# Kernel tuning notes

Hardware: AMD Instinct MI355X
Metric: run time of the kernel (lower is better)

The kernel has to match this reference:

```python
import jax, jax.numpy as jnp
import numpy as np

B, LEADS, T = 256, 12, 2250
ENC_DIM = 768           # encoder.width
LATENT = 128            # latent_dim
K = 512                 # num_embeddings
COMMIT = 0.1            # commitment_cost
IN_DIM = LEADS * T      # 27000


def setup_inputs() -> dict:
    key = jax.random.key(0)
    ks = jax.random.split(key, 9)
    s = lambda d: 1.0 / np.sqrt(d)
    return {
        "x": jax.random.normal(ks[0], (B, LEADS, T), dtype=jnp.float32),
        # frozen pretrained encoder, modeled as a linear projection (stop_gradient in reference)
        "W_enc": jax.random.normal(ks[1], (IN_DIM, ENC_DIM), dtype=jnp.float32) * s(IN_DIM),
        # to_latent
        "W_lat": jax.random.normal(ks[2], (ENC_DIM, LATENT), dtype=jnp.float32) * s(ENC_DIM),
        "b_lat": jnp.zeros((LATENT,), dtype=jnp.float32),
        # VQ codebook: torch.rand - 0.5  -> uniform(-0.5, 0.5)
        "codebook": jax.random.uniform(ks[3], (K, LATENT), dtype=jnp.float32, minval=-0.5, maxval=0.5),
        # decoder: Linear(LATENT, ENC_DIM) -> ReLU -> Linear(ENC_DIM, IN_DIM)
        "W_d1": jax.random.normal(ks[4], (LATENT, ENC_DIM), dtype=jnp.float32) * s(LATENT),
        "b_d1": jnp.zeros((ENC_DIM,), dtype=jnp.float32),
        "W_d2": jax.random.normal(ks[5], (ENC_DIM, IN_DIM), dtype=jnp.float32) * s(ENC_DIM),
        "b_d2": jnp.zeros((IN_DIM,), dtype=jnp.float32),
    }


def _vq(z, codebook):
    # z: [B, D]; codebook: [K, D]
    # distances = |z|^2 + |e|^2 - 2 z e^T   -> [B, K]
    d = (jnp.sum(z * z, axis=1, keepdims=True)
         + jnp.sum(codebook * codebook, axis=1)
         - 2.0 * jnp.matmul(z, codebook.T))
    idx = jnp.argmin(d, axis=1)                 # [B]
    quant = codebook[idx]                       # gather [B, D]
    e_latent = jnp.mean((jax.lax.stop_gradient(quant) - z) ** 2)
    q_latent = jnp.mean((quant - jax.lax.stop_gradient(z)) ** 2)
    loss = q_latent + COMMIT * e_latent
    quant_st = z + jax.lax.stop_gradient(quant - z)   # straight-through
    return quant_st, loss, idx


def reference(x, W_enc, W_lat, b_lat, codebook, W_d1, b_d1, W_d2, b_d2):
    # frozen encoder (requires_grad=False / torch.no_grad)
    features = jax.lax.stop_gradient(x.reshape(x.shape[0], -1) @ W_enc)   # [B, ENC_DIM]
    z = features @ W_lat + b_lat                                          # [B, LATENT]
    z_q, vq_loss, indices = _vq(z, codebook)
    h = jax.nn.relu(z_q @ W_d1 + b_d1)
    x_recon = (h @ W_d2 + b_d2).reshape(-1, LEADS, T)                     # [B, 12, 2250]
    recon_loss = jnp.mean((x_recon - x) ** 2)
    return x_recon, recon_loss + vq_loss, vq_loss, indices
```

## Files before the change

kernel.cpp:

```cpp
#include <hip/hip_runtime.h>
#include <hip/hip_bf16.h>

#define IN_DIM   27000
#define ENC_DIM  768
#define LATENT   128
#define K_CODES  512
#define BATCH    256
#define ZCH      288
#define NZC      94
#define NWC      422
#define BN_R     64
#define NRB      422
#define PADK     40
#define NKT      24

#define OUT_WCTH_US   0
#define OUT_WCTL_US   (128*IN_DIM)
#define OUT_ZPART_F   (128*IN_DIM)

#define WS_Z      0
#define WS_QUANT  (WS_Z + BATCH*LATENT)
#define WS_IDX    (WS_QUANT + BATCH*LATENT)
#define WS_VQPART (WS_IDX + BATCH)
#define WS_RECON  (WS_VQPART + BATCH)
#define WS_HBF    (WS_RECON + 1024)
#define WS_WLH    (WS_HBF + 49152)
#define WS_WLL    (WS_WLH + 49152)

typedef unsigned short ushort_t;
typedef __attribute__((ext_vector_type(4))) float f32x4;
typedef __attribute__((ext_vector_type(8))) short short8x;
typedef __attribute__((ext_vector_type(4))) short short4x;

__device__ __forceinline__ ushort_t bf16_rne(float f) {
    unsigned u = __float_as_uint(f);
    unsigned r = 0x7FFFu + ((u >> 16) & 1u);
    return (ushort_t)((u + r) >> 16);
}
__device__ __forceinline__ void split_f32(float v, ushort_t& h, ushort_t& l) {
    unsigned u  = __float_as_uint(v);
    unsigned uh = u & 0xFFFF0000u;
    h = (ushort_t)(uh >> 16);
    l = bf16_rne(v - __uint_as_float(uh));
}
__device__ __forceinline__ void lds_barrier() {
    asm volatile("s_waitcnt lgkmcnt(0)\n\ts_barrier" ::: "memory");
}

__global__ __launch_bounds__(256) void k_prep(const float* __restrict__ Wlat,
                                              ushort_t* __restrict__ wlh,
                                              ushort_t* __restrict__ wll) {
    const int i4 = blockIdx.x * 256 + threadIdx.x;
    const int k  = i4 >> 5;
    const int n4 = (i4 & 31) * 4;
    float4 v = *(const float4*)(Wlat + (size_t)k * LATENT + n4);
    float vv[4] = {v.x, v.y, v.z, v.w};
#pragma unroll
    for (int j = 0; j < 4; j++) {
        ushort_t h, l;
        split_f32(vv[j], h, l);
        wlh[(size_t)(n4 + j) * ENC_DIM + k] = h;
        wll[(size_t)(n4 + j) * ENC_DIM + k] = l;
    }
}

__global__ __launch_bounds__(256) void k_wc(const float* __restrict__ Wenc,
                                            const ushort_t* __restrict__ wlh,
                                            const ushort_t* __restrict__ wll,
                                            ushort_t* __restrict__ wcth,
                                            ushort_t* __restrict__ wctl) {
    __shared__ ushort_t Ah[2][64][PADK], Al[2][64][PADK];
    __shared__ ushort_t Bh[2][128][PADK], Bl[2][128][PADK];
    const int t = threadIdx.x, lane = t & 63, w = t >> 6;
    const int lrow = lane & 15, kg = lane >> 4;
    const int m0 = blockIdx.x * 64;

    const int a_row = t >> 3, a_kq = t & 7;
    const int b_n   = t >> 2, b_ck = t & 3;

    float4  areg0[2], areg1[2];
    short8x bhreg0[2], blreg0[2], bhreg1[2], blreg1[2];

    f32x4 acc[8];
#pragma unroll
    for (int ni = 0; ni < 8; ni++) acc[ni] = (f32x4){0.f, 0.f, 0.f, 0.f};

#define WC_LOAD(S, kt)                                                          \
    {                                                                           \
        const int k0_ = (kt) * 32;                                              \
        _Pragma("unroll")                                                       \
        for (int p = 0; p < 2; p++) {                                           \
            int r = m0 + a_row + p * 32; if (r > IN_DIM - 1) r = IN_DIM - 1;    \
            areg##S[p] = *(const float4*)(Wenc + (size_t)r * ENC_DIM + k0_ + a_kq * 4); \
        }                                                                       \
        _Pragma("unroll")                                                       \
        for (int p = 0; p < 2; p++) {                                           \
            const size_t bo = (size_t)(b_n + p * 64) * ENC_DIM + k0_ + b_ck * 8;\
            bhreg##S[p] = *(const short8x*)(wlh + bo);                          \
            blreg##S[p] = *(const short8x*)(wll + bo);                          \
        }                                                                       \
    }
#define WC_STORE(S, BI)                                                         \
    {                                                                           \
        _Pragma("unroll")                                                       \
        for (int p = 0; p < 2; p++) {                                           \
            const int row = a_row + p * 32;                                     \
            float vv[4] = {areg##S[p].x, areg##S[p].y, areg##S[p].z, areg##S[p].w}; \
            short4x h4, l4;                                                     \
            _Pragma("unroll")                                                   \
            for (int i = 0; i < 4; i++) {                                       \
                ushort_t h, l; split_f32(vv[i], h, l);                          \
                h4[i] = (short)h; l4[i] = (short)l;                             \
            }                                                                   \
            *(short4x*)&Ah[BI][row][a_kq * 4] = h4;                             \
            *(short4x*)&Al[BI][row][a_kq * 4] = l4;                             \
        }                                                                       \
        _Pragma("unroll")                                                       \
        for (int p = 0; p < 2; p++) {                                           \
            const int n = b_n + p * 64;                                         \
            *(short8x*)&Bh[BI][n][b_ck * 8] = bhreg##S[p];                      \
            *(short8x*)&Bl[BI][n][b_ck * 8] = blreg##S[p];                      \
        }                                                                       \
    }
#define WC_MFMA(BI)                                                             \
    {                                                                           \
        short8x ah = *(const short8x*)&Ah[BI][w * 16 + lrow][kg * 8];           \
        short8x al = *(const short8x*)&Al[BI][w * 16 + lrow][kg * 8];           \
        _Pragma("unroll")                                                       \
        for (int ni = 0; ni < 8; ni++) {                                        \
            short8x bhf = *(const short8x*)&Bh[BI][ni * 16 + lrow][kg * 8];     \
            short8x blf = *(const short8x*)&Bl[BI][ni * 16 + lrow][kg * 8];     \
            acc[ni] = __builtin_amdgcn_mfma_f32_16x16x32_bf16(ah, bhf, acc[ni], 0, 0, 0); \
            acc[ni] = __builtin_amdgcn_mfma_f32_16x16x32_bf16(ah, blf, acc[ni], 0, 0, 0); \
            acc[ni] = __builtin_amdgcn_mfma_f32_16x16x32_bf16(al, bhf, acc[ni], 0, 0, 0); \
        }                                                                       \
    }

    const int NT = NKT;
    WC_LOAD(0, 0)
    WC_LOAD(1, 1)
    WC_STORE(0, 0)
    lds_barrier();

    for (int kt = 0; kt < NT; kt += 2) {
        if (kt + 2 < NT) WC_LOAD(0, kt + 2)
        WC_MFMA(0)
        WC_STORE(1, 1)
        lds_barrier();
        if (kt + 3 < NT) WC_LOAD(1, kt + 3)
        WC_MFMA(1)
        if (kt + 2 < NT) WC_STORE(0, 0)
        lds_barrier();
    }
#undef WC_LOAD
#undef WC_STORE
#undef WC_MFMA

    const int rowb = m0 + w * 16 + kg * 4;
    if (rowb < IN_DIM) {
#pragma unroll
        for (int ni = 0; ni < 8; ni++) {
            const int col = ni * 16 + lrow;
            short4x h4, l4;
#pragma unroll
            for (int r = 0; r < 4; r++) {
                ushort_t h, l; split_f32(acc[ni][r], h, l);
                h4[r] = (short)h; l4[r] = (short)l;
            }
            *(short4x*)(wcth + (size_t)col * IN_DIM + rowb) = h4;
            *(short4x*)(wctl + (size_t)col * IN_DIM + rowb) = l4;
        }
    }
}

__global__ __launch_bounds__(256) void k_z(const float* __restrict__ x,
                                           const ushort_t* __restrict__ wcth,
                                           const ushort_t* __restrict__ wctl,
                                           float* __restrict__ zpart) {
    __shared__ ushort_t Ah[2][64][PADK], Al[2][64][PADK];
    __shared__ ushort_t Bh[2][128][PADK], Bl[2][128][PADK];
    const int t = threadIdx.x, lane = t & 63, w = t >> 6;
    const int lrow = lane & 15, kg = lane >> 4;
    const int m0 = blockIdx.x * 64;
    const int c  = blockIdx.y;
    const int kb = c * ZCH;
    const int k_end = min(IN_DIM, kb + ZCH);
    const int nt = (k_end - kb + 31) >> 5;

    const int a_row = t >> 3, a_kq = t & 7;
    const int b_n   = t >> 2, b_ck = t & 3;

    float4  areg0[2], areg1[2];
    short8x bhreg0[2], blreg0[2], bhreg1[2], blreg1[2];

    f32x4 acc[8];
#pragma unroll
    for (int ni = 0; ni < 8; ni++) acc[ni] = (f32x4){0.f, 0.f, 0.f, 0.f};

#define Z_LOAD(S, kt)                                                           \
    {                                                                           \
        const int k0_ = kb + (kt) * 32;                                         \
        _Pragma("unroll")                                                       \
        for (int p = 0; p < 2; p++) {                                           \
            const int kk = k0_ + a_kq * 4;                                      \
            if (kk < k_end) {                                                   \
                const int r = m0 + a_row + p * 32;                              \
                areg##S[p] = *(const float4*)(x + (size_t)r * IN_DIM + kk);     \
            } else {                                                            \
                areg##S[p] = (float4){0.f, 0.f, 0.f, 0.f};                      \
            }                                                                   \
        }                                                                       \
        _Pragma("unroll")                                                       \
        for (int p = 0; p < 2; p++) {                                           \
            const int kk = k0_ + b_ck * 8;                                      \
            if (kk < k_end) {                                                   \
                const size_t bo = (size_t)(b_n + p * 64) * IN_DIM + kk;         \
                bhreg##S[p] = *(const short8x*)(wcth + bo);                     \
                blreg##S[p] = *(const short8x*)(wctl + bo);                     \
            } else {                                                            \
                short8x zz = {0, 0, 0, 0, 0, 0, 0, 0};                          \
                bhreg##S[p] = zz; blreg##S[p] = zz;                             \
            }                                                                   \
        }                                                                       \
    }
#define Z_STORE(S, BI)                                                          \
    {                                                                           \
        _Pragma("unroll")                                                       \
        for (int p = 0; p < 2; p++) {                                           \
            const int row = a_row + p * 32;                                     \
            float vv[4] = {areg##S[p].x, areg##S[p].y, areg##S[p].z, areg##S[p].w}; \
            short4x h4, l4;                                                     \
            _Pragma("unroll")                                                   \
            for (int i = 0; i < 4; i++) {                                       \
                ushort_t h, l; split_f32(vv[i], h, l);                          \
                h4[i] = (short)h; l4[i] = (short)l;                             \
            }                                                                   \
            *(short4x*)&Ah[BI][row][a_kq * 4] = h4;                             \
            *(short4x*)&Al[BI][row][a_kq * 4] = l4;                             \
        }                                                                       \
        _Pragma("unroll")                                                       \
        for (int p = 0; p < 2; p++) {                                           \
            const int n = b_n + p * 64;                                         \
            *(short8x*)&Bh[BI][n][b_ck * 8] = bhreg##S[p];                      \
            *(short8x*)&Bl[BI][n][b_ck * 8] = blreg##S[p];                      \
        }                                                                       \
    }
#define Z_MFMA(BI)                                                              \
    {                                                                           \
        short8x ah = *(const short8x*)&Ah[BI][w * 16 + lrow][kg * 8];           \
        short8x al = *(const short8x*)&Al[BI][w * 16 + lrow][kg * 8];           \
        _Pragma("unroll")                                                       \
        for (int ni = 0; ni < 8; ni++) {                                        \
            short8x bhf = *(const short8x*)&Bh[BI][ni * 16 + lrow][kg * 8];     \
            short8x blf = *(const short8x*)&Bl[BI][ni * 16 + lrow][kg * 8];     \
            acc[ni] = __builtin_amdgcn_mfma_f32_16x16x32_bf16(ah, bhf, acc[ni], 0, 0, 0); \
            acc[ni] = __builtin_amdgcn_mfma_f32_16x16x32_bf16(ah, blf, acc[ni], 0, 0, 0); \
            acc[ni] = __builtin_amdgcn_mfma_f32_16x16x32_bf16(al, bhf, acc[ni], 0, 0, 0); \
        }                                                                       \
    }

    Z_LOAD(0, 0)
    if (nt > 1) Z_LOAD(1, 1)
    Z_STORE(0, 0)
    lds_barrier();

    for (int kt = 0; kt < nt; kt += 2) {
        if (kt + 2 < nt) Z_LOAD(0, kt + 2)
        Z_MFMA(0)
        if (kt + 1 < nt) Z_STORE(1, 1)
        lds_barrier();
        if (kt + 1 < nt) {
            if (kt + 3 < nt) Z_LOAD(1, kt + 3)
            Z_MFMA(1)
            if (kt + 2 < nt) Z_STORE(0, 0)
            lds_barrier();
        }
    }
#undef Z_LOAD
#undef Z_STORE
#undef Z_MFMA

    float* zp = zpart + (size_t)c * (BATCH * LATENT);
    const int rowb = m0 + w * 16 + kg * 4;
#pragma unroll
    for (int ni = 0; ni < 8; ni++) {
        const int col = ni * 16 + lrow;
#pragma unroll
        for (int r = 0; r < 4; r++)
            zp[(size_t)(rowb + r) * LATENT + col] = acc[ni][r];
    }
}

__global__ __launch_bounds__(256) void k_zred(const float* __restrict__ zpart,
                                              const float* __restrict__ blat,
                                              float* __restrict__ z) {
    const int o = blockIdx.x * 256 + threadIdx.x;
    float s = blat[o & (LATENT - 1)];
    for (int c = 0; c < NZC; c++) s += zpart[(size_t)c * (BATCH * LATENT) + o];
    z[o] = s;
}

__global__ __launch_bounds__(256) void k_vq(const float* __restrict__ z,
                                            const float* __restrict__ cb,
                                            float* __restrict__ quant,
                                            int* __restrict__ idx_out,
                                            float* __restrict__ vqpart) {
    __shared__ float zs[LATENT];
    __shared__ float ds_[256];
    __shared__ int   is_[256];
    const int b = blockIdx.x, t = threadIdx.x;
    if (t < LATENT) zs[t] = z[b * LATENT + t];
    __syncthreads();

    float best_d = 3.4e38f; int best_i = 0;
#pragma unroll
    for (int rep = 0; rep < 2; rep++) {
        const int k = t + rep * 256;
        const float* e = cb + (size_t)k * LATENT;
        float acc = 0.f;
#pragma unroll 4
        for (int d = 0; d < LATENT; d += 4) {
            float4 ev = *(const float4*)(e + d);
            float d0 = zs[d]   - ev.x;
            float d1 = zs[d+1] - ev.y;
            float d2 = zs[d+2] - ev.z;
            float d3 = zs[d+3] - ev.w;
            acc += d0*d0 + d1*d1 + d2*d2 + d3*d3;
        }
        if (acc < best_d) { best_d = acc; best_i = k; }
    }
    ds_[t] = best_d; is_[t] = best_i;
    __syncthreads();
    for (int s = 128; s > 0; s >>= 1) {
        if (t < s) {
            float od = ds_[t+s]; int oi = is_[t+s];
            if (od < ds_[t] || (od == ds_[t] && oi < is_[t])) { ds_[t] = od; is_[t] = oi; }
        }
        __syncthreads();
    }
    const int best = is_[0];
    if (t == 0) idx_out[b] = best;

    float sq = 0.f;
    if (t < LATENT) {
        float q = cb[(size_t)best * LATENT + t];
        quant[b * LATENT + t] = q;
        float dd = q - zs[t];
        sq = dd * dd;
    }
    __syncthreads();
    ds_[t] = sq;
    __syncthreads();
    for (int s = 128; s > 0; s >>= 1) {
        if (t < s) ds_[t] += ds_[t+s];
        __syncthreads();
    }
    if (t == 0) vqpart[b] = ds_[0];
}

__global__ __launch_bounds__(256) void k_h(const float* __restrict__ quant,
                                           const float* __restrict__ Wd1,
                                           const float* __restrict__ bd1,
                                           ushort_t* __restrict__ hfrag) {
    const int bid = blockIdx.x, t = threadIdx.x;
    const int row = bid / 3;
    const int col = (bid % 3) * 256 + t;
    float acc = bd1[col];
    const float* q = quant + row * LATENT;
#pragma unroll 8
    for (int k = 0; k < LATENT; k++)
        acc = fmaf(q[k], Wd1[(size_t)k * ENC_DIM + col], acc);
    const int mt = row >> 4, lrow = row & 15;
    const int kt = col >> 5, kg = (col & 31) >> 3, j = col & 7;
    hfrag[((size_t)(mt * NKT + kt) * 64 + kg * 16 + lrow) * 8 + j] =
        bf16_rne(fmaxf(acc, 0.f));
}

__global__ __launch_bounds__(512) void k_recon_mfma(const ushort_t* __restrict__ hfrag,
                                                    const float* __restrict__ Wd2,
                                                    const float* __restrict__ bd2,
                                                    const float* __restrict__ x,
                                                    float* __restrict__ out,
                                                    float* __restrict__ reconpart) {
    __shared__ ushort_t Bts[2][BN_R][PADK];
    __shared__ float red[512];
    const int t = threadIdx.x, lane = t & 63, wid = t >> 6;
    const int lrow = lane & 15, kg = lane >> 4;
    const int n0 = blockIdx.x * BN_R;

    const int b_n   = lane;
    const int b_kq  = wid;
    const bool bvalid = (n0 + b_n) < IN_DIM;
    const ushort_t* afrag0 = hfrag + ((size_t)(wid * 2 + 0) * NKT * 64 + lane) * 8;
    const ushort_t* afrag1 = hfrag + ((size_t)(wid * 2 + 1) * NKT * 64 + lane) * 8;

    f32x4 acc[2][4];
#pragma unroll
    for (int mi = 0; mi < 2; mi++)
#pragma unroll
        for (int ni = 0; ni < 4; ni++) acc[mi][ni] = (f32x4){0.f, 0.f, 0.f, 0.f};

    short8x a0[2], a1[2], a2[2], a3[2];
    float   bregs0[4], bregs1[4], bregs2[4], bregs3[4];

#define R_ALOAD(S, kt)                                                          \
    {                                                                           \
        a##S[0] = *(const short8x*)(afrag0 + (size_t)(kt) * 512);               \
        a##S[1] = *(const short8x*)(afrag1 + (size_t)(kt) * 512);               \
    }
#define R_BLOAD(S, kt)                                                          \
    {                                                                           \
        if (bvalid) {                                                           \
            const float* wp = Wd2 + (size_t)((kt) * 32 + b_kq * 4) * IN_DIM + n0 + b_n; \
            _Pragma("unroll")                                                   \
            for (int j = 0; j < 4; j++) bregs##S[j] = wp[(size_t)j * IN_DIM];   \
        } else {                                                                \
            _Pragma("unroll")                                                   \
            for (int j = 0; j < 4; j++) bregs##S[j] = 0.f;                      \
        }                                                                       \
    }
#define R_BSTORE(S, BI)                                                         \
    {                                                                           \
        short4x bb;                                                             \
        _Pragma("unroll")                                                       \
        for (int j = 0; j < 4; j++) bb[j] = (short)bf16_rne(bregs##S[j]);       \
        *(short4x*)&Bts[BI][b_n][b_kq * 4] = bb;                                \
    }
#define R_MFMA(S, BI)                                                           \
    {                                                                           \
        short8x b_[4];                                                          \
        _Pragma("unroll")                                                       \
        for (int ni = 0; ni < 4; ni++)                                          \
            b_[ni] = *(const short8x*)&Bts[BI][ni * 16 + lrow][kg * 8];         \
        _Pragma("unroll")                                                       \
        for (int mi = 0; mi < 2; mi++)                                          \
            _Pragma("unroll")                                                   \
            for (int ni = 0; ni < 4; ni++)                                      \
                acc[mi][ni] = __builtin_amdgcn_mfma_f32_16x16x32_bf16(a##S[mi], b_[ni], acc[mi][ni], 0, 0, 0); \
    }

    R_ALOAD(0, 0) R_BLOAD(0, 0)
    R_ALOAD(1, 1) R_BLOAD(1, 1)
    R_ALOAD(2, 2) R_BLOAD(2, 2)
    R_BSTORE(0, 0)
    lds_barrier();

    for (int kt0 = 0; kt0 < NKT; kt0 += 4) {
        if (kt0 + 3 < NKT) { R_ALOAD(3, kt0 + 3) R_BLOAD(3, kt0 + 3) }
        R_MFMA(0, 0)
        if (kt0 + 1 < NKT) R_BSTORE(1, 1)
        lds_barrier();
        if (kt0 + 4 < NKT) { R_ALOAD(0, kt0 + 4) R_BLOAD(0, kt0 + 4) }
        R_MFMA(1, 1)
        if (kt0 + 2 < NKT) R_BSTORE(2, 0)
        lds_barrier();
        if (kt0 + 5 < NKT) { R_ALOAD(1, kt0 + 5) R_BLOAD(1, kt0 + 5) }
        R_MFMA(2, 0)
        if (kt0 + 3 < NKT) R_BSTORE(3, 1)
        lds_barrier();
        if (kt0 + 6 < NKT) { R_ALOAD(2, kt0 + 6) R_BLOAD(2, kt0 + 6) }
        R_MFMA(3, 1)
        if (kt0 + 4 < NKT) R_BSTORE(0, 0)
        lds_barrier();
    }
#undef R_ALOAD
#undef R_BLOAD
#undef R_BSTORE
#undef R_MFMA

    float lsq = 0.f;
#pragma unroll
    for (int mi = 0; mi < 2; mi++) {
        const int rowb = wid * 32 + mi * 16 + kg * 4;
#pragma unroll
        for (int ni = 0; ni < 4; ni++) {
            const int col = n0 + ni * 16 + lrow;
            if (col < IN_DIM) {
                const float bb = bd2[col];
#pragma unroll
                for (int r = 0; r < 4; r++) {
                    const int row = rowb + r;
                    float v = acc[mi][ni][r] + bb;
                    float e = v - x[(size_t)row * IN_DIM + col];
                    lsq += e * e;
                    out[(size_t)row * IN_DIM + col] = v;
                }
            }
        }
    }

    red[t] = lsq;
    __syncthreads();
    for (int s = 256; s > 0; s >>= 1) {
        if (t < s) red[t] += red[t + s];
        __syncthreads();
    }
    if (t == 0) reconpart[blockIdx.x] = red[0];
}

__global__ __launch_bounds__(256) void k_final(const float* __restrict__ reconpart,
                                               const float* __restrict__ vqpart,
                                               const int* __restrict__ idx,
                                               float* __restrict__ out,
                                               long long obase) {
    __shared__ float red[256];
    const int t = threadIdx.x;
    float s = 0.f;
    for (int i = t; i < NRB; i += 256) s += reconpart[i];
    red[t] = s;
    __syncthreads();
    for (int st = 128; st > 0; st >>= 1) {
        if (t < st) red[t] += red[t + st];
        __syncthreads();
    }
    const float recon_sum = red[0];
    __syncthreads();
    red[t] = vqpart[t];
    __syncthreads();
    for (int st = 128; st > 0; st >>= 1) {
        if (t < st) red[t] += red[t + st];
        __syncthreads();
    }
    const float vq_sum = red[0];
    if (t == 0) {
        float recon_loss = recon_sum / (float)((size_t)BATCH * IN_DIM);
        float vq_loss = 1.1f * vq_sum / (float)(BATCH * LATENT);
        out[obase + 0] = recon_loss + vq_loss;
        out[obase + 1] = vq_loss;
    }
    out[obase + 2 + t] = (float)idx[t];
}

extern "C" void kernel_launch(void* const* d_in, const int* in_sizes, int n_in,
                              void* d_out, int out_size, void* d_ws, size_t ws_size,
                              hipStream_t stream) {
    int ix = 0, iwe = 1, iwl = 2, ibl = 3, icb = 4, iwd1 = 5, ibd1 = 6, iwd2 = 7, ibd2 = 8;
    if (n_in == 9 && in_sizes[0] != BATCH * IN_DIM) {
        int p20[2] = {1, 7}, n20 = 0, p98[2] = {2, 5}, n98 = 0;
        for (int i = 0; i < 9; i++) {
            const int s = in_sizes[i];
            if      (s == BATCH * IN_DIM)    ix = i;
            else if (s == LATENT)            ibl = i;
            else if (s == K_CODES * LATENT)  icb = i;
            else if (s == ENC_DIM)           ibd1 = i;
            else if (s == IN_DIM)            ibd2 = i;
            else if (s == IN_DIM * ENC_DIM)  { if (n20 < 2) p20[n20++] = i; }
            else if (s == ENC_DIM * LATENT)  { if (n98 < 2) p98[n98++] = i; }
        }
        iwd2 = p20[0]; iwe = p20[1];
        iwd1 = p98[0]; iwl = p98[1];
    }
    const float* x    = (const float*)d_in[ix];
    const float* Wenc = (const float*)d_in[iwe];
    const float* Wlat = (const float*)d_in[iwl];
    const float* blat = (const float*)d_in[ibl];
    const float* cb   = (const float*)d_in[icb];
    const float* Wd1  = (const float*)d_in[iwd1];
    const float* bd1  = (const float*)d_in[ibd1];
    const float* Wd2  = (const float*)d_in[iwd2];
    const float* bd2  = (const float*)d_in[ibd2];

    float* out = (float*)d_out;
    ushort_t* wcth  = (ushort_t*)d_out + OUT_WCTH_US;
    ushort_t* wctl  = (ushort_t*)d_out + OUT_WCTL_US;
    float*    zpart = out + OUT_ZPART_F;

    float* ws            = (float*)d_ws;
    float* z             = ws + WS_Z;
    float* quant         = ws + WS_QUANT;
    int*   idxp          = (int*)(ws + WS_IDX);
    float* vqpart        = ws + WS_VQPART;
    float* reconpart     = ws + WS_RECON;
    ushort_t* hfrag      = (ushort_t*)(ws + WS_HBF);
    ushort_t* wlh        = (ushort_t*)(ws + WS_WLH);
    ushort_t* wll        = (ushort_t*)(ws + WS_WLL);

    const long long obase = (long long)out_size - 258;

    k_prep      <<<96, 256, 0, stream>>>(Wlat, wlh, wll);
    k_wc        <<<NWC, 256, 0, stream>>>(Wenc, wlh, wll, wcth, wctl);
    k_z         <<<dim3(4, NZC), 256, 0, stream>>>(x, wcth, wctl, zpart);
    k_zred      <<<128, 256, 0, stream>>>(zpart, blat, z);
    k_vq        <<<BATCH, 256, 0, stream>>>(z, cb, quant, idxp, vqpart);
    k_h         <<<768, 256, 0, stream>>>(quant, Wd1, bd1, hfrag);
    k_recon_mfma<<<NRB, 512, 0, stream>>>(hfrag, Wd2, bd2, x, out, reconpart);
    k_final     <<<1, 256, 0, stream>>>(reconpart, vqpart, idxp, out, obase);
}
```

Before: 128.8 us.

## Load A operand directly into MFMA registers, skipping LDS staging in k_wc and k_z

In both the W_enc×W_lat precompute kernel and the x×Wc GEMM, the A operand (fp32 rows) is now read straight from global memory into the per-lane MFMA fragment layout and split to bf16 hi/lo in registers, instead of being staged through shared memory. A is prefetched three k-tiles ahead with a 4-deep register ring, while B keeps double-buffered LDS staging. This removes the A LDS writes and reads and halves shared memory use, at the cost of more registers and less coalesced per-lane global loads (32 contiguous bytes per lane).

```diff
diff --git a/kernel.cpp b/kernel.cpp
--- a/kernel.cpp
+++ b/kernel.cpp
@@ -69,63 +69,49 @@
                                             const ushort_t* __restrict__ wll,
                                             ushort_t* __restrict__ wcth,
                                             ushort_t* __restrict__ wctl) {
-    __shared__ ushort_t Ah[2][64][PADK], Al[2][64][PADK];
     __shared__ ushort_t Bh[2][128][PADK], Bl[2][128][PADK];
     const int t = threadIdx.x, lane = t & 63, w = t >> 6;
     const int lrow = lane & 15, kg = lane >> 4;
     const int m0 = blockIdx.x * 64;
-
-    const int a_row = t >> 3, a_kq = t & 7;
-    const int b_n   = t >> 2, b_ck = t & 3;
-
-    float4  areg0[2], areg1[2];
-    short8x bhreg0[2], blreg0[2], bhreg1[2], blreg1[2];
+    int arow = m0 + w * 16 + lrow; if (arow > IN_DIM - 1) arow = IN_DIM - 1;
+    const float* aptr = Wenc + (size_t)arow * ENC_DIM + kg * 8;
+    const int bn = t >> 1, bkc = (t & 1) * 16;
+    const size_t bbase = (size_t)bn * ENC_DIM + bkc;
 
     f32x4 acc[8];
 #pragma unroll
     for (int ni = 0; ni < 8; ni++) acc[ni] = (f32x4){0.f, 0.f, 0.f, 0.f};
 
-#define WC_LOAD(S, kt)                                                          \
-    {                                                                           \
-        const int k0_ = (kt) * 32;                                              \
-        _Pragma("unroll")                                                       \
-        for (int p = 0; p < 2; p++) {                                           \
-            int r = m0 + a_row + p * 32; if (r > IN_DIM - 1) r = IN_DIM - 1;    \
-            areg##S[p] = *(const float4*)(Wenc + (size_t)r * ENC_DIM + k0_ + a_kq * 4); \
+    float av0[8], av1[8], av2[8], av3[8];
+    short8x bh0[2], bl0[2], bh1[2], bl1[2];
+
+#define WC_ALOAD(S, kt)                                                         \
+    {                                                                           \
+        *(float4*)&av##S[0] = *(const float4*)(aptr + (kt) * 32);               \
+        *(float4*)&av##S[4] = *(const float4*)(aptr + (kt) * 32 + 4);           \
+    }
+#define WC_BLOAD(S, kt)                                                         \
+    {                                                                           \
+        const ushort_t* ph = wlh + bbase + (kt) * 32;                           \
+        const ushort_t* pl = wll + bbase + (kt) * 32;                           \
+        bh##S[0] = *(const short8x*)ph;   bh##S[1] = *(const short8x*)(ph + 8); \
+        bl##S[0] = *(const short8x*)pl;   bl##S[1] = *(const short8x*)(pl + 8); \
+    }
+#define WC_BSTORE(S, BI)                                                        \
+    {                                                                           \
+        *(short8x*)&Bh[BI][bn][bkc]     = bh##S[0];                             \
+        *(short8x*)&Bh[BI][bn][bkc + 8] = bh##S[1];                             \
+        *(short8x*)&Bl[BI][bn][bkc]     = bl##S[0];                             \
+        *(short8x*)&Bl[BI][bn][bkc + 8] = bl##S[1];                             \
+    }
+#define WC_MFMA(S, BI)                                                          \
+    {                                                                           \
+        short8x ah, al;                                                         \
+        _Pragma("unroll")                                                       \
+        for (int i = 0; i < 8; i++) {                                           \
+            ushort_t h, l; split_f32(av##S[i], h, l);                           \
+            ah[i] = (short)h; al[i] = (short)l;                                 \
         }                                                                       \
-        _Pragma("unroll")                                                       \
-        for (int p = 0; p < 2; p++) {                                           \
-            const size_t bo = (size_t)(b_n + p * 64) * ENC_DIM + k0_ + b_ck * 8;\
-            bhreg##S[p] = *(const short8x*)(wlh + bo);                          \
-            blreg##S[p] = *(const short8x*)(wll + bo);                          \
-        }                                                                       \
-    }
-#define WC_STORE(S, BI)                                                         \
-    {                                                                           \
-        _Pragma("unroll")                                                       \
-        for (int p = 0; p < 2; p++) {                                           \
-            const int row = a_row + p * 32;                                     \
-            float vv[4] = {areg##S[p].x, areg##S[p].y, areg##S[p].z, areg##S[p].w}; \
-            short4x h4, l4;                                                     \
-            _Pragma("unroll")                                                   \
-            for (int i = 0; i < 4; i++) {                                       \
-                ushort_t h, l; split_f32(vv[i], h, l);                          \
-                h4[i] = (short)h; l4[i] = (short)l;                             \
-            }                                                                   \
-            *(short4x*)&Ah[BI][row][a_kq * 4] = h4;                             \
-            *(short4x*)&Al[BI][row][a_kq * 4] = l4;                             \
-        }                                                                       \
-        _Pragma("unroll")                                                       \
-        for (int p = 0; p < 2; p++) {                                           \
-            const int n = b_n + p * 64;                                         \
-            *(short8x*)&Bh[BI][n][b_ck * 8] = bhreg##S[p];                      \
-            *(short8x*)&Bl[BI][n][b_ck * 8] = blreg##S[p];                      \
-        }                                                                       \
-    }
-#define WC_MFMA(BI)                                                             \
-    {                                                                           \
-        short8x ah = *(const short8x*)&Ah[BI][w * 16 + lrow][kg * 8];           \
-        short8x al = *(const short8x*)&Al[BI][w * 16 + lrow][kg * 8];           \
         _Pragma("unroll")                                                       \
         for (int ni = 0; ni < 8; ni++) {                                        \
             short8x bhf = *(const short8x*)&Bh[BI][ni * 16 + lrow][kg * 8];     \
@@ -136,24 +122,36 @@
         }                                                                       \
     }
 
-    const int NT = NKT;
-    WC_LOAD(0, 0)
-    WC_LOAD(1, 1)
-    WC_STORE(0, 0)
+    WC_ALOAD(0, 0) WC_ALOAD(1, 1) WC_ALOAD(2, 2)
+    WC_BLOAD(0, 0) WC_BLOAD(1, 1)
+    WC_BSTORE(0, 0)
     lds_barrier();
 
-    for (int kt = 0; kt < NT; kt += 2) {
-        if (kt + 2 < NT) WC_LOAD(0, kt + 2)
-        WC_MFMA(0)
-        WC_STORE(1, 1)
-        lds_barrier();
-        if (kt + 3 < NT) WC_LOAD(1, kt + 3)
-        WC_MFMA(1)
-        if (kt + 2 < NT) WC_STORE(0, 0)
-        lds_barrier();
-    }
-#undef WC_LOAD
-#undef WC_STORE
+    for (int kt0 = 0; kt0 < NKT; kt0 += 4) {
+        if (kt0 + 3 < NKT) WC_ALOAD(3, kt0 + 3)
+        if (kt0 + 2 < NKT) WC_BLOAD(0, kt0 + 2)
+        WC_MFMA(0, 0)
+        if (kt0 + 1 < NKT) WC_BSTORE(1, 1)
+        lds_barrier();
+        if (kt0 + 4 < NKT) WC_ALOAD(0, kt0 + 4)
+        if (kt0 + 3 < NKT) WC_BLOAD(1, kt0 + 3)
+        WC_MFMA(1, 1)
+        if (kt0 + 2 < NKT) WC_BSTORE(0, 0)
+        lds_barrier();
+        if (kt0 + 5 < NKT) WC_ALOAD(1, kt0 + 5)
+        if (kt0 + 4 < NKT) WC_BLOAD(0, kt0 + 4)
+        WC_MFMA(2, 0)
+        if (kt0 + 3 < NKT) WC_BSTORE(1, 1)
+        lds_barrier();
+        if (kt0 + 6 < NKT) WC_ALOAD(2, kt0 + 6)
+        if (kt0 + 5 < NKT) WC_BLOAD(1, kt0 + 5)
+        WC_MFMA(3, 1)
+        if (kt0 + 4 < NKT) WC_BSTORE(0, 0)
+        lds_barrier();
+    }
+#undef WC_ALOAD
+#undef WC_BLOAD
+#undef WC_BSTORE
 #undef WC_MFMA
 
     const int rowb = m0 + w * 16 + kg * 4;
@@ -177,7 +175,6 @@
                                            const ushort_t* __restrict__ wcth,
                                            const ushort_t* __restrict__ wctl,
                                            float* __restrict__ zpart) {
-    __shared__ ushort_t Ah[2][64][PADK], Al[2][64][PADK];
     __shared__ ushort_t Bh[2][128][PADK], Bl[2][128][PADK];
     const int t = threadIdx.x, lane = t & 63, w = t >> 6;
     const int lrow = lane & 15, kg = lane >> 4;
@@ -187,68 +184,55 @@
     const int k_end = min(IN_DIM, kb + ZCH);
     const int nt = (k_end - kb + 31) >> 5;
 
-    const int a_row = t >> 3, a_kq = t & 7;
-    const int b_n   = t >> 2, b_ck = t & 3;
-
-    float4  areg0[2], areg1[2];
-    short8x bhreg0[2], blreg0[2], bhreg1[2], blreg1[2];
+    const float* aptr = x + (size_t)(m0 + w * 16 + lrow) * IN_DIM + kb + kg * 8;
+    const int bn = t >> 1, bkc = (t & 1) * 16;
+    const size_t bbase = (size_t)bn * IN_DIM + kb + bkc;
 
     f32x4 acc[8];
 #pragma unroll
     for (int ni = 0; ni < 8; ni++) acc[ni] = (f32x4){0.f, 0.f, 0.f, 0.f};
 
-#define Z_LOAD(S, kt)                                                           \
-    {                                                                           \
-        const int k0_ = kb + (kt) * 32;                                         \
-        _Pragma("unroll")                                                       \
-        for (int p = 0; p < 2; p++) {                                           \
-            const int kk = k0_ + a_kq * 4;                                      \
-            if (kk < k_end) {                                                   \
-                const int r = m0 + a_row + p * 32;                              \
-                areg##S[p] = *(const float4*)(x + (size_t)r * IN_DIM + kk);     \
-            } else {                                                            \
-                areg##S[p] = (float4){0.f, 0.f, 0.f, 0.f};                      \
-            }                                                                   \
+    float av0[8], av1[8], av2[8], av3[8];
+    short8x bh0[2], bl0[2], bh1[2], bl1[2];
+
+#define Z_ALOAD(S, kt)                                                          \
+    {                                                                           \
+        if (kb + (kt) * 32 + kg * 8 < k_end) {                                  \
+            *(float4*)&av##S[0] = *(const float4*)(aptr + (kt) * 32);           \
+            *(float4*)&av##S[4] = *(const float4*)(aptr + (kt) * 32 + 4);       \
+        } else {                                                                \
+            _Pragma("unroll")                                                   \
+            for (int i = 0; i < 8; i++) av##S[i] = 0.f;                         \
         }                                                                       \
-        _Pragma("unroll")                                                       \
-        for (int p = 0; p < 2; p++) {                                           \
-            const int kk = k0_ + b_ck * 8;                                      \
-            if (kk < k_end) {                                                   \
-                const size_t bo = (size_t)(b_n + p * 64) * IN_DIM + kk;         \
-                bhreg##S[p] = *(const short8x*)(wcth + bo);                     \
-                blreg##S[p] = *(const short8x*)(wctl + bo);                     \
-            } else {                                                            \
-                short8x zz = {0, 0, 0, 0, 0, 0, 0, 0};                          \
-                bhreg##S[p] = zz; blreg##S[p] = zz;                             \
-            }                                                                   \
+    }
+#define Z_BLOAD(S, kt)                                                          \
+    {                                                                           \
+        const int ko = kb + (kt) * 32 + bkc;                                    \
+        const ushort_t* ph = wcth + bbase + (kt) * 32;                          \
+        const ushort_t* pl = wctl + bbase + (kt) * 32;                          \
+        const short8x zz = {0, 0, 0, 0, 0, 0, 0, 0};                            \
+        if (ko < k_end)     { bh##S[0] = *(const short8x*)ph;                   \
+                              bl##S[0] = *(const short8x*)pl; }                 \
+        else                { bh##S[0] = zz; bl##S[0] = zz; }                   \
+        if (ko + 8 < k_end) { bh##S[1] = *(const short8x*)(ph + 8);             \
+                              bl##S[1] = *(const short8x*)(pl + 8); }           \
+        else                { bh##S[1] = zz; bl##S[1] = zz; }                   \
+    }
+#define Z_BSTORE(S, BI)                                                         \
+    {                                                                           \
+        *(short8x*)&Bh[BI][bn][bkc]     = bh##S[0];                             \
+        *(short8x*)&Bh[BI][bn][bkc + 8] = bh##S[1];                             \
+        *(short8x*)&Bl[BI][bn][bkc]     = bl##S[0];                             \
+        *(short8x*)&Bl[BI][bn][bkc + 8] = bl##S[1];                             \
+    }
+#define Z_MFMA(S, BI)                                                           \
+    {                                                                           \
+        short8x ah, al;                                                         \
+        _Pragma("unroll")                                                       \
+        for (int i = 0; i < 8; i++) {                                           \
+            ushort_t h, l; split_f32(av##S[i], h, l);                           \
+            ah[i] = (short)h; al[i] = (short)l;                                 \
         }                                                                       \
-    }
-#define Z_STORE(S, BI)                                                          \
-    {                                                                           \
-        _Pragma("unroll")                                                       \
-        for (int p = 0; p < 2; p++) {                                           \
-            const int row = a_row + p * 32;                                     \
-            float vv[4] = {areg##S[p].x, areg##S[p].y, areg##S[p].z, areg##S[p].w}; \
-            short4x h4, l4;                                                     \
-            _Pragma("unroll")                                                   \
-            for (int i = 0; i < 4; i++) {                                       \
-                ushort_t h, l; split_f32(vv[i], h, l);                          \
-                h4[i] = (short)h; l4[i] = (short)l;                             \
-            }                                                                   \
-            *(short4x*)&Ah[BI][row][a_kq * 4] = h4;                             \
-            *(short4x*)&Al[BI][row][a_kq * 4] = l4;                             \
-        }                                                                       \
-        _Pragma("unroll")                                                       \
-        for (int p = 0; p < 2; p++) {                                           \
-            const int n = b_n + p * 64;                                         \
-            *(short8x*)&Bh[BI][n][b_ck * 8] = bhreg##S[p];                      \
-            *(short8x*)&Bl[BI][n][b_ck * 8] = blreg##S[p];                      \
-        }                                                                       \
-    }
-#define Z_MFMA(BI)                                                              \
-    {                                                                           \
-        short8x ah = *(const short8x*)&Ah[BI][w * 16 + lrow][kg * 8];           \
-        short8x al = *(const short8x*)&Al[BI][w * 16 + lrow][kg * 8];           \
         _Pragma("unroll")                                                       \
         for (int ni = 0; ni < 8; ni++) {                                        \
             short8x bhf = *(const short8x*)&Bh[BI][ni * 16 + lrow][kg * 8];     \
@@ -259,25 +243,44 @@
         }                                                                       \
     }
 
-    Z_LOAD(0, 0)
-    if (nt > 1) Z_LOAD(1, 1)
-    Z_STORE(0, 0)
+    Z_ALOAD(0, 0) Z_ALOAD(1, 1) Z_ALOAD(2, 2)
+    Z_BLOAD(0, 0) Z_BLOAD(1, 1)
+    Z_BSTORE(0, 0)
     lds_barrier();
 
-    for (int kt = 0; kt < nt; kt += 2) {
-        if (kt + 2 < nt) Z_LOAD(0, kt + 2)
-        Z_MFMA(0)
-        if (kt + 1 < nt) Z_STORE(1, 1)
-        lds_barrier();
-        if (kt + 1 < nt) {
-            if (kt + 3 < nt) Z_LOAD(1, kt + 3)
-            Z_MFMA(1)
-            if (kt + 2 < nt) Z_STORE(0, 0)
+    for (int kt0 = 0; kt0 < nt; kt0 += 4) {
+        if (kt0 + 0 < nt) {
+            if (kt0 + 3 < nt) Z_ALOAD(3, kt0 + 3)
+            if (kt0 + 2 < nt) Z_BLOAD(0, kt0 + 2)
+            Z_MFMA(0, 0)
+            if (kt0 + 1 < nt) Z_BSTORE(1, 1)
             lds_barrier();
         }
-    }
-#undef Z_LOAD
-#undef Z_STORE
+        if (kt0 + 1 < nt) {
+            if (kt0 + 4 < nt) Z_ALOAD(0, kt0 + 4)
+            if (kt0 + 3 < nt) Z_BLOAD(1, kt0 + 3)
+            Z_MFMA(1, 1)
+            if (kt0 + 2 < nt) Z_BSTORE(0, 0)
+            lds_barrier();
+        }
+        if (kt0 + 2 < nt) {
+            if (kt0 + 5 < nt) Z_ALOAD(1, kt0 + 5)
+            if (kt0 + 4 < nt) Z_BLOAD(0, kt0 + 4)
+            Z_MFMA(2, 0)
+            if (kt0 + 3 < nt) Z_BSTORE(1, 1)
+            lds_barrier();
+        }
+        if (kt0 + 3 < nt) {
+            if (kt0 + 6 < nt) Z_ALOAD(2, kt0 + 6)
+            if (kt0 + 5 < nt) Z_BLOAD(1, kt0 + 5)
+            Z_MFMA(3, 1)
+            if (kt0 + 4 < nt) Z_BSTORE(0, 0)
+            lds_barrier();
+        }
+    }
+#undef Z_ALOAD
+#undef Z_BLOAD
+#undef Z_BSTORE
 #undef Z_MFMA
 
     float* zp = zpart + (size_t)c * (BATCH * LATENT);
```

Measured after the change: 133.1 us. 1.03x slower.

## Load W_enc A-fragments directly to registers in k_wc and raise MFMA priority

Applied to the files above, without the earlier changes.

The k_wc kernel no longer stages the W_enc tile through LDS. Each lane loads its own A fragment straight from global memory into registers, splits it into bf16 hi/lo just before the MFMAs, and keeps a 4-deep register prefetch of A while B stays double-buffered in LDS. This removes the A-tile LDS traffic and its split-and-store work, at the cost of more registers and less coalesced per-lane A loads. s_setprio(1) is also wrapped around the MFMA blocks in three GEMM kernels so waves issuing MFMAs get scheduling priority over waves issuing loads.

```diff
diff --git a/kernel.cpp b/kernel.cpp
--- a/kernel.cpp
+++ b/kernel.cpp
@@ -69,63 +69,50 @@
                                             const ushort_t* __restrict__ wll,
                                             ushort_t* __restrict__ wcth,
                                             ushort_t* __restrict__ wctl) {
-    __shared__ ushort_t Ah[2][64][PADK], Al[2][64][PADK];
     __shared__ ushort_t Bh[2][128][PADK], Bl[2][128][PADK];
     const int t = threadIdx.x, lane = t & 63, w = t >> 6;
     const int lrow = lane & 15, kg = lane >> 4;
     const int m0 = blockIdx.x * 64;
-
-    const int a_row = t >> 3, a_kq = t & 7;
-    const int b_n   = t >> 2, b_ck = t & 3;
-
-    float4  areg0[2], areg1[2];
-    short8x bhreg0[2], blreg0[2], bhreg1[2], blreg1[2];
+    int arow = m0 + w * 16 + lrow; if (arow > IN_DIM - 1) arow = IN_DIM - 1;
+    const float* aptr = Wenc + (size_t)arow * ENC_DIM + kg * 8;
+    const int bn = t >> 1, bkc = (t & 1) * 16;
+    const size_t bbase = (size_t)bn * ENC_DIM + bkc;
 
     f32x4 acc[8];
 #pragma unroll
     for (int ni = 0; ni < 8; ni++) acc[ni] = (f32x4){0.f, 0.f, 0.f, 0.f};
 
-#define WC_LOAD(S, kt)                                                          \
-    {                                                                           \
-        const int k0_ = (kt) * 32;                                              \
-        _Pragma("unroll")                                                       \
-        for (int p = 0; p < 2; p++) {                                           \
-            int r = m0 + a_row + p * 32; if (r > IN_DIM - 1) r = IN_DIM - 1;    \
-            areg##S[p] = *(const float4*)(Wenc + (size_t)r * ENC_DIM + k0_ + a_kq * 4); \
-        }                                                                       \
-        _Pragma("unroll")                                                       \
-        for (int p = 0; p < 2; p++) {                                           \
-            const size_t bo = (size_t)(b_n + p * 64) * ENC_DIM + k0_ + b_ck * 8;\
-            bhreg##S[p] = *(const short8x*)(wlh + bo);                          \
-            blreg##S[p] = *(const short8x*)(wll + bo);                          \
-        }                                                                       \
-    }
-#define WC_STORE(S, BI)                                                         \
-    {                                                                           \
-        _Pragma("unroll")                                                       \
-        for (int p = 0; p < 2; p++) {                                           \
-            const int row = a_row + p * 32;                                     \
-            float vv[4] = {areg##S[p].x, areg##S[p].y, areg##S[p].z, areg##S[p].w}; \
-            short4x h4, l4;                                                     \
-            _Pragma("unroll")                                                   \
-            for (int i = 0; i < 4; i++) {                                       \
-                ushort_t h, l; split_f32(vv[i], h, l);                          \
-                h4[i] = (short)h; l4[i] = (short)l;                             \
-            }                                                                   \
-            *(short4x*)&Ah[BI][row][a_kq * 4] = h4;                             \
-            *(short4x*)&Al[BI][row][a_kq * 4] = l4;                             \
-        }                                                                       \
-        _Pragma("unroll")                                                       \
-        for (int p = 0; p < 2; p++) {                                           \
-            const int n = b_n + p * 64;                                         \
-            *(short8x*)&Bh[BI][n][b_ck * 8] = bhreg##S[p];                      \
-            *(short8x*)&Bl[BI][n][b_ck * 8] = blreg##S[p];                      \
-        }                                                                       \
-    }
-#define WC_MFMA(BI)                                                             \
-    {                                                                           \
-        short8x ah = *(const short8x*)&Ah[BI][w * 16 + lrow][kg * 8];           \
-        short8x al = *(const short8x*)&Al[BI][w * 16 + lrow][kg * 8];           \
+    float av0[8], av1[8], av2[8], av3[8];
+    short8x bh0[2], bl0[2], bh1[2], bl1[2];
+
+#define WC_ALOAD(S, kt)                                                         \
+    {                                                                           \
+        *(float4*)&av##S[0] = *(const float4*)(aptr + (kt) * 32);               \
+        *(float4*)&av##S[4] = *(const float4*)(aptr + (kt) * 32 + 4);           \
+    }
+#define WC_BLOAD(S, kt)                                                         \
+    {                                                                           \
+        const ushort_t* ph = wlh + bbase + (kt) * 32;                           \
+        const ushort_t* pl = wll + bbase + (kt) * 32;                           \
+        bh##S[0] = *(const short8x*)ph;   bh##S[1] = *(const short8x*)(ph + 8); \
+        bl##S[0] = *(const short8x*)pl;   bl##S[1] = *(const short8x*)(pl + 8); \
+    }
+#define WC_BSTORE(S, BI)                                                        \
+    {                                                                           \
+        *(short8x*)&Bh[BI][bn][bkc]     = bh##S[0];                             \
+        *(short8x*)&Bh[BI][bn][bkc + 8] = bh##S[1];                             \
+        *(short8x*)&Bl[BI][bn][bkc]     = bl##S[0];                             \
+        *(short8x*)&Bl[BI][bn][bkc + 8] = bl##S[1];                             \
+    }
+#define WC_MFMA(S, BI)                                                          \
+    {                                                                           \
+        short8x ah, al;                                                         \
+        _Pragma("unroll")                                                       \
+        for (int i = 0; i < 8; i++) {                                           \
+            ushort_t h, l; split_f32(av##S[i], h, l);                           \
+            ah[i] = (short)h; al[i] = (short)l;                                 \
+        }                                                                       \
+        __builtin_amdgcn_s_setprio(1);                                          \
         _Pragma("unroll")                                                       \
         for (int ni = 0; ni < 8; ni++) {                                        \
             short8x bhf = *(const short8x*)&Bh[BI][ni * 16 + lrow][kg * 8];     \
@@ -134,26 +121,39 @@
             acc[ni] = __builtin_amdgcn_mfma_f32_16x16x32_bf16(ah, blf, acc[ni], 0, 0, 0); \
             acc[ni] = __builtin_amdgcn_mfma_f32_16x16x32_bf16(al, bhf, acc[ni], 0, 0, 0); \
         }                                                                       \
-    }
-
-    const int NT = NKT;
-    WC_LOAD(0, 0)
-    WC_LOAD(1, 1)
-    WC_STORE(0, 0)
+        __builtin_amdgcn_s_setprio(0);                                          \
+    }
+
+    WC_ALOAD(0, 0) WC_ALOAD(1, 1) WC_ALOAD(2, 2)
+    WC_BLOAD(0, 0) WC_BLOAD(1, 1)
+    WC_BSTORE(0, 0)
     lds_barrier();
 
-    for (int kt = 0; kt < NT; kt += 2) {
-        if (kt + 2 < NT) WC_LOAD(0, kt + 2)
-        WC_MFMA(0)
-        WC_STORE(1, 1)
-        lds_barrier();
-        if (kt + 3 < NT) WC_LOAD(1, kt + 3)
-        WC_MFMA(1)
-        if (kt + 2 < NT) WC_STORE(0, 0)
-        lds_barrier();
-    }
-#undef WC_LOAD
-#undef WC_STORE
+    for (int kt0 = 0; kt0 < NKT; kt0 += 4) {
+        if (kt0 + 3 < NKT) WC_ALOAD(3, kt0 + 3)
+        if (kt0 + 2 < NKT) WC_BLOAD(0, kt0 + 2)
+        WC_MFMA(0, 0)
+        if (kt0 + 1 < NKT) WC_BSTORE(1, 1)
+        lds_barrier();
+        if (kt0 + 4 < NKT) WC_ALOAD(0, kt0 + 4)
+        if (kt0 + 3 < NKT) WC_BLOAD(1, kt0 + 3)
+        WC_MFMA(1, 1)
+        if (kt0 + 2 < NKT) WC_BSTORE(0, 0)
+        lds_barrier();
+        if (kt0 + 5 < NKT) WC_ALOAD(1, kt0 + 5)
+        if (kt0 + 4 < NKT) WC_BLOAD(0, kt0 + 4)
+        WC_MFMA(2, 0)
+        if (kt0 + 3 < NKT) WC_BSTORE(1, 1)
+        lds_barrier();
+        if (kt0 + 6 < NKT) WC_ALOAD(2, kt0 + 6)
+        if (kt0 + 5 < NKT) WC_BLOAD(1, kt0 + 5)
+        WC_MFMA(3, 1)
+        if (kt0 + 4 < NKT) WC_BSTORE(0, 0)
+        lds_barrier();
+    }
+#undef WC_ALOAD
+#undef WC_BLOAD
+#undef WC_BSTORE
 #undef WC_MFMA
 
     const int rowb = m0 + w * 16 + kg * 4;
@@ -249,6 +249,7 @@
     {                                                                           \
         short8x ah = *(const short8x*)&Ah[BI][w * 16 + lrow][kg * 8];           \
         short8x al = *(const short8x*)&Al[BI][w * 16 + lrow][kg * 8];           \
+        __builtin_amdgcn_s_setprio(1);                                          \
         _Pragma("unroll")                                                       \
         for (int ni = 0; ni < 8; ni++) {                                        \
             short8x bhf = *(const short8x*)&Bh[BI][ni * 16 + lrow][kg * 8];     \
@@ -257,6 +258,7 @@
             acc[ni] = __builtin_amdgcn_mfma_f32_16x16x32_bf16(ah, blf, acc[ni], 0, 0, 0); \
             acc[ni] = __builtin_amdgcn_mfma_f32_16x16x32_bf16(al, bhf, acc[ni], 0, 0, 0); \
         }                                                                       \
+        __builtin_amdgcn_s_setprio(0);                                          \
     }
 
     Z_LOAD(0, 0)
@@ -432,11 +434,13 @@
         _Pragma("unroll")                                                       \
         for (int ni = 0; ni < 4; ni++)                                          \
             b_[ni] = *(const short8x*)&Bts[BI][ni * 16 + lrow][kg * 8];         \
+        __builtin_amdgcn_s_setprio(1);                                          \
         _Pragma("unroll")                                                       \
         for (int mi = 0; mi < 2; mi++)                                          \
             _Pragma("unroll")                                                   \
             for (int ni = 0; ni < 4; ni++)                                      \
                 acc[mi][ni] = __builtin_amdgcn_mfma_f32_16x16x32_bf16(a##S[mi], b_[ni], acc[mi][ni], 0, 0, 0); \
+        __builtin_amdgcn_s_setprio(0);                                          \
     }
 
     R_ALOAD(0, 0) R_BLOAD(0, 0)
```

Measured after the change: 129.9 us. About the same (+0.8%).
